# Kernel optimization log

Measured on AMD Instinct MI355X. Metric: run time of the kernel, lower is better.

Reference implementation:

```python
import jax, jax.numpy as jnp
import numpy as np

PHI = (1.0 + float(np.sqrt(5.0))) / 2.0  # golden ratio used by the model


def setup_inputs() -> dict:
    key = jax.random.key(0)
    ks = jax.random.split(key, 12)
    B, S = 4, 1024
    V, D, H, N = 32000, 128, 8, 128
    dh = D // H
    return {
        'input_ids': jax.random.randint(ks[0], (B, S), 0, V),
        'emb': jax.random.normal(ks[1], (V, 2 * D), jnp.float32),
        'w_query': jax.random.normal(ks[2], (H, dh), jnp.float32) * 0.02,
        'b_query': jnp.zeros((H, dh), jnp.float32),
        'w_key': jax.random.normal(ks[3], (H, dh), jnp.float32) * 0.02,
        'b_key': jnp.zeros((H, dh), jnp.float32),
        'W_ctx': jax.random.normal(ks[4], (D, D), jnp.float32) * 0.05,
        'W_res': jax.random.normal(ks[5], (N, D), jnp.float32) * 0.02,
        'B_res': jnp.zeros((N, D), jnp.float32),
        'W_real': jax.random.normal(ks[6], (D, N), jnp.float32) * 0.05,
        'W_imag': jax.random.normal(ks[7], (D, N), jnp.float32) * 0.05,
        'W_out': jax.random.normal(ks[8], (V, D), jnp.float32) * 0.02,
    }


def _forward(input_ids, emb, w_query, b_query, w_key, b_key,
             W_ctx, W_res, B_res, W_real, W_imag, W_out):
    B, S = input_ids.shape
    D = W_ctx.shape[0]
    H, dh = w_query.shape
    e = emb[input_ids]                      # [B,S,2D]
    w_emb, b_emb = e[..., :D], e[..., D:]
    t = jnp.arange(S, dtype=jnp.float32)    # time indices
    tphi = t * PHI

    # --- sequential Euler recurrence (independent of attention) -> states X ---
    def step(carry, xs):
        h_r, h_i = carry
        w_t, b_t, tp = xs                   # w_t,b_t: [B,D]; tp: scalar
        wl = 1.0 + jnp.abs(w_t)
        th_r = h_r / wl + b_t + tp
        th_i = h_i / wl + b_t + tp
        sr, cr = jnp.sin(th_r), jnp.cos(th_r)
        si, ci = jnp.sin(th_i), jnp.cos(th_i)
        new_r = cr * ci - sr * si
        new_i = cr * si + sr * ci
        return (new_r, new_i), new_r + new_i

    init = (jnp.zeros((B, D), e.dtype), jnp.zeros((B, D), e.dtype))
    _, Xs = jax.lax.scan(step, init, (jnp.swapaxes(w_emb, 0, 1),
                                      jnp.swapaxes(b_emb, 0, 1), tphi))
    X = jnp.swapaxes(Xs, 0, 1)              # [B,S,D] cached states

    # --- multi-head Euler-phase attention with strict-causal (exclusive) mask ---
    Xh = X.reshape(B, S, H, dh)
    th_q = Xh / (1.0 + jnp.abs(w_query)) + b_query + tphi[None, :, None, None]
    q = jnp.concatenate([jnp.cos(th_q), jnp.sin(th_q)], axis=-1)   # [B,S,H,2dh]
    th_k = Xh / (1.0 + jnp.abs(w_key)) + b_key                     # keys: no t term
    k = jnp.concatenate([jnp.cos(th_k), jnp.sin(th_k)], axis=-1)
    scores = jnp.einsum('bihd,bjhd->bhij', q, k) / jnp.sqrt(2.0 * dh)
    mask = jnp.tril(jnp.ones((S, S), bool), k=-1)                  # j < i strictly
    scores = jnp.where(mask, scores, -1e9)
    wts = jax.nn.softmax(scores, axis=-1) * mask                   # row 0 -> all-zero
    context = jnp.einsum('bhij,bjd->bid', wts, X)                  # heads summed
    x = X + context @ W_ctx.T

    # --- resonant trig layer ---
    theta = x[:, :, None, :] / (1.0 + jnp.abs(W_res)) + B_res \
            + tphi[None, :, None, None]                            # [B,S,N,D]
    cos_sum = jnp.cos(theta).sum(-1)                               # [B,S,N]
    sin_sum = jnp.sin(theta).sum(-1)
    x = x + jax.nn.silu(cos_sum @ W_real.T + sin_sum @ W_imag.T)

    return x @ W_out.T                                             # [B,S,V]


def reference(input_ids, emb, w_query, b_query, w_key, b_key,
              W_ctx, W_res, B_res, W_real, W_imag, W_out):
    return _forward(input_ids, emb, w_query, b_query, w_key, b_key,
                    W_ctx, W_res, B_res, W_real, W_imag, W_out)
```

## Files before the change

kernel.cpp:

```cpp
#include <hip/hip_runtime.h>


#define DEV static __device__ __forceinline__

typedef __attribute__((ext_vector_type(8))) short short8;
typedef __attribute__((ext_vector_type(4))) float f32x4;

#define INV2PI 0.15915494309189535f
#define INVPI  0.3183098861837907f
#define PHI    1.6180339887498949f
#define SSCALE 0.17677669529663687f

DEV unsigned short f2bf(float x){
  unsigned u = __float_as_uint(x);
  u += 0x7fff + ((u >> 16) & 1);
  return (unsigned short)(u >> 16);
}
DEV float fract1(float x){ return __builtin_amdgcn_fractf(x); }
DEV float sin2pi(float f){ return __builtin_amdgcn_sinf(f); }
DEV float cos2pi(float f){ return __builtin_amdgcn_cosf(f); }
DEV float rcpf_(float x){ return __builtin_amdgcn_rcpf(x); }

DEV void cp16(const float* g, float* l){
  __builtin_amdgcn_global_load_lds(
      (const __attribute__((address_space(1))) unsigned*)g,
      (__attribute__((address_space(3))) unsigned*)l, 16, 0, 0);
}

__global__ __launch_bounds__(256) void k_cast(
    const float* __restrict__ Wctx, const float* __restrict__ Wres,
    const float* __restrict__ Bres, const float* __restrict__ Wreal,
    const float* __restrict__ Wimag, const float* __restrict__ Wout,
    unsigned short* __restrict__ Woutb, unsigned short* __restrict__ Wctxb,
    unsigned short* __restrict__ WriTb, float* __restrict__ raT,
    float* __restrict__ rcT){
  int i = blockIdx.x * 256 + threadIdx.x;
  if (i < 4096000){ Woutb[i] = f2bf(Wout[i]); return; }
  i -= 4096000;
  if (i < 16384){ Wctxb[i] = f2bf(Wctx[i]); return; }
  i -= 16384;
  if (i < 32768){
    int d = i >> 8, kk = i & 255;
    WriTb[i] = f2bf(kk < 128 ? Wreal[d*128 + kk] : Wimag[d*128 + kk - 128]);
    return;
  }
  i -= 32768;
  if (i < 16384){
    int d = i >> 7, n = i & 127;
    raT[i] = INV2PI * rcpf_(1.f + fabsf(Wres[n*128 + d]));
    rcT[i] = Bres[n*128 + d] * INV2PI;
  }
}

__global__ __launch_bounds__(128) void k_prep(const int* __restrict__ ids,
    const float* __restrict__ emb, float* __restrict__ P){
  int bt = blockIdx.x;
  int t  = bt & 1023;
  int d  = threadIdx.x;
  int id = ids[bt];
  float w  = emb[id*256 + d];
  float bb = emb[id*256 + 128 + d];
  float a = INV2PI * rcpf_(1.f + fabsf(w));
  float c = (bb + (float)t * PHI) * INVPI;
  ((float2*)P)[bt*128 + d] = make_float2(a, c);
}

__global__ __launch_bounds__(128) void k_scan(const float* __restrict__ P,
                                              float* __restrict__ X,
                                              unsigned short* __restrict__ XT){
  __shared__ float buf[2][32*256];
  int b  = blockIdx.x;
  int tid = threadIdx.x;
  int wv = tid >> 6, ln = tid & 63;
  const float* Pb = P + (size_t)b * 1024 * 256;
  for (int i = 0; i < 16; i++){
    int o = (i*2 + wv) * 256;
    cp16(Pb + o + ln*4, &buf[0][o]);
  }
  __syncthreads();
  float s = 0.f;
  float* Xb = X + (size_t)b * 1024 * 128;
  unsigned short* XTb = XT + (size_t)(b*128 + tid) * 1024;
  for (int c = 0; c < 32; c++){
    int cur = c & 1;
    if (c + 1 < 32){
      const float* Pn = Pb + (size_t)(c+1) * 8192;
      float* lb = &buf[cur ^ 1][0];
      for (int i = 0; i < 16; i++){
        int o = (i*2 + wv) * 256;
        cp16(Pn + o + ln*4, lb + o);
      }
    }
    const float* bc = &buf[cur][0];
    unsigned pk[16];
    #pragma unroll
    for (int t = 0; t < 32; t++){
      float a  = bc[t*256 + tid*2];
      float cc = bc[t*256 + tid*2 + 1];
      float rev = fmaf(s, a, cc);
      float f = fract1(rev);
      s = sin2pi(f) + cos2pi(f);
      Xb[(c*32 + t)*128 + tid] = s;
      unsigned short h = f2bf(s);
      if (t & 1) pk[t>>1] |= (unsigned)h << 16;
      else       pk[t>>1]  = (unsigned)h;
    }
    uint4* dst = (uint4*)(XTb + c*32);
    #pragma unroll
    for (int i = 0; i < 4; i++)
      dst[i] = make_uint4(pk[i*4+0], pk[i*4+1], pk[i*4+2], pk[i*4+3]);
    __syncthreads();
  }
}

__global__ __launch_bounds__(128) void k_qk(const float* __restrict__ X,
    const float* __restrict__ wq, const float* __restrict__ bq,
    const float* __restrict__ wk, const float* __restrict__ bk,
    unsigned short* __restrict__ q, unsigned short* __restrict__ k){
  int bt = blockIdx.x;
  int t = bt & 1023;
  int tid = threadIdx.x;
  float x = X[(size_t)bt*128 + tid];
  int h = tid >> 4, c = tid & 15;
  size_t base = (size_t)bt*256 + h*32 + c;
  float aq = rcpf_(1.f + fabsf(wq[tid]));
  float fq = fract1(fmaf(x, aq, bq[tid] + (float)t * PHI) * INV2PI);
  q[base]      = f2bf(cos2pi(fq));
  q[base + 16] = f2bf(sin2pi(fq));
  float ak = rcpf_(1.f + fabsf(wk[tid]));
  float fk = fract1(fmaf(x, ak, bk[tid]) * INV2PI);
  k[base]      = f2bf(cos2pi(fk));
  k[base + 16] = f2bf(sin2pi(fk));
}

__global__ __launch_bounds__(256) void k_attn_z(const unsigned short* __restrict__ q,
    const unsigned short* __restrict__ k, float* __restrict__ Z){
  int blk = blockIdx.x;
  int it = blk & 15, h = (blk >> 4) & 7, b = blk >> 7;
  int tid = threadIdx.x, w = tid >> 6, ln = tid & 63;
  int ib = it*64 + w*16;
  short8 qa = *(const short8*)(q + ((size_t)(b*1024 + ib + (ln & 15))*8 + h)*32 + (ln >> 4)*8);
  const unsigned short* kb = k + ((size_t)(b*1024 + (ln & 15))*8 + h)*32 + (ln >> 4)*8;
  float z0 = 0.f, z1 = 0.f, z2 = 0.f, z3 = 0.f;
  int irow = ib + (ln >> 4)*4;
  int jcol = ln & 15;
  for (int jt = 0; jt <= (ib >> 4); jt++){
    short8 kf = *(const short8*)(kb + (size_t)jt*16*256);
    f32x4 c = {0.f, 0.f, 0.f, 0.f};
    c = __builtin_amdgcn_mfma_f32_16x16x32_bf16(qa, kf, c, 0, 0, 0);
    int j = jt*16 + jcol;
    if (j < irow + 0) z0 += __expf(c[0]*SSCALE);
    if (j < irow + 1) z1 += __expf(c[1]*SSCALE);
    if (j < irow + 2) z2 += __expf(c[2]*SSCALE);
    if (j < irow + 3) z3 += __expf(c[3]*SSCALE);
  }
  #pragma unroll
  for (int m = 1; m < 16; m <<= 1){
    z0 += __shfl_xor(z0, m, 64); z1 += __shfl_xor(z1, m, 64);
    z2 += __shfl_xor(z2, m, 64); z3 += __shfl_xor(z3, m, 64);
  }
  if ((ln & 15) == 0){
    float* zp = Z + (size_t)(b*8 + h)*1024 + irow;
    zp[0] = z0; zp[1] = z1; zp[2] = z2; zp[3] = z3;
  }
}

__global__ __launch_bounds__(256) void k_attn_w(const unsigned short* __restrict__ q,
    const unsigned short* __restrict__ k, const float* __restrict__ Z,
    unsigned short* __restrict__ W){
  __shared__ float invZ[8][64];
  int b = blockIdx.x / 136, tr = blockIdx.x % 136;
  int it = 0; while ((it+1)*(it+2)/2 <= tr) it++;
  int jt = tr - it*(it+1)/2;
  int ib = it*64, jb = jt*64;
  int tid = threadIdx.x;
  for (int i = tid; i < 512; i += 256){
    int hh = i >> 6, rr = i & 63;
    float zz = Z[(size_t)(b*8 + hh)*1024 + ib + rr];
    invZ[hh][rr] = zz > 0.f ? rcpf_(zz) : 0.f;
  }
  __syncthreads();
  int w = tid >> 6, ln = tid & 63;
  int iw = ib + w*16;
  int rloc = w*16 + (ln >> 4)*4;
  int irow = iw + (ln >> 4)*4;
  int jcol = ln & 15;
  float acc[4][4] = {};
  for (int h = 0; h < 8; h++){
    short8 qa = *(const short8*)(q + ((size_t)(b*1024 + iw + (ln & 15))*8 + h)*32 + (ln >> 4)*8);
    float iz0 = invZ[h][rloc+0], iz1 = invZ[h][rloc+1];
    float iz2 = invZ[h][rloc+2], iz3 = invZ[h][rloc+3];
    for (int jtt = 0; jtt < 4; jtt++){
      short8 kf = *(const short8*)(k + ((size_t)(b*1024 + jb + jtt*16 + (ln & 15))*8 + h)*32 + (ln >> 4)*8);
      f32x4 c = {0.f, 0.f, 0.f, 0.f};
      c = __builtin_amdgcn_mfma_f32_16x16x32_bf16(qa, kf, c, 0, 0, 0);
      int j = jb + jtt*16 + jcol;
      if (j < irow + 0) acc[jtt][0] += __expf(c[0]*SSCALE)*iz0;
      if (j < irow + 1) acc[jtt][1] += __expf(c[1]*SSCALE)*iz1;
      if (j < irow + 2) acc[jtt][2] += __expf(c[2]*SSCALE)*iz2;
      if (j < irow + 3) acc[jtt][3] += __expf(c[3]*SSCALE)*iz3;
    }
  }
  #pragma unroll
  for (int jtt = 0; jtt < 4; jtt++)
    #pragma unroll
    for (int r = 0; r < 4; r++)
      W[(size_t)(b*1024 + irow + r)*1024 + jb + jtt*16 + jcol] = f2bf(acc[jtt][r]);
}

__global__ __launch_bounds__(256) void k_gemm(const unsigned short* __restrict__ A,
    const unsigned short* __restrict__ B, void* __restrict__ Cv,
    int K, int lda, int ldb, int ldc,
    long Abat, long Bbat, long Cbat, int causal, int obf,
    const float* __restrict__ Xadd){
  int bz = blockIdx.z;
  A += (long)bz * Abat; B += (long)bz * Bbat;
  int tid = threadIdx.x, w = tid >> 6, ln = tid & 63;
  int m0 = blockIdx.x*128 + (w & 1)*64;
  int n0 = blockIdx.y*128 + (w >> 1)*64;
  int kmax = causal ? (blockIdx.x + 1)*128 : K;
  if (kmax > K) kmax = K;
  f32x4 acc[4][4];
  #pragma unroll
  for (int i = 0; i < 4; i++)
    #pragma unroll
    for (int j = 0; j < 4; j++) acc[i][j] = (f32x4){0.f, 0.f, 0.f, 0.f};
  const unsigned short* Ap = A + (long)(m0 + (ln & 15))*lda + (ln >> 4)*8;
  const unsigned short* Bp = B + (long)(n0 + (ln & 15))*ldb + (ln >> 4)*8;
  for (int kb = 0; kb < kmax; kb += 32){
    short8 af[4], bf[4];
    #pragma unroll
    for (int i = 0; i < 4; i++) af[i] = *(const short8*)(Ap + (long)i*16*lda + kb);
    #pragma unroll
    for (int i = 0; i < 4; i++) bf[i] = *(const short8*)(Bp + (long)i*16*ldb + kb);
    #pragma unroll
    for (int i = 0; i < 4; i++)
      #pragma unroll
      for (int j = 0; j < 4; j++)
        acc[i][j] = __builtin_amdgcn_mfma_f32_16x16x32_bf16(af[i], bf[j], acc[i][j], 0, 0, 0);
  }
  int r0 = (ln >> 4)*4, jc = ln & 15;
  if (obf == 1){
    unsigned short* C = (unsigned short*)Cv + (long)bz * Cbat;
    #pragma unroll
    for (int i = 0; i < 4; i++)
      #pragma unroll
      for (int j = 0; j < 4; j++)
        #pragma unroll
        for (int r = 0; r < 4; r++)
          C[(long)(m0 + i*16 + r0 + r)*ldc + n0 + j*16 + jc] = f2bf(acc[i][j][r]);
  } else if (obf == 2){
    unsigned short* C = (unsigned short*)Cv;
    #pragma unroll
    for (int i = 0; i < 4; i++)
      #pragma unroll
      for (int j = 0; j < 4; j++)
        #pragma unroll
        for (int r = 0; r < 4; r++){
          long idx = (long)(m0 + i*16 + r0 + r)*ldc + n0 + j*16 + jc;
          float uu = acc[i][j][r];
          float sig = rcpf_(1.f + __expf(-uu));
          C[idx] = f2bf(Xadd[idx] + uu*sig);
        }
  } else if (obf == 3){
    float* C = (float*)Cv + (long)bz * Cbat;
    #pragma unroll
    for (int i = 0; i < 4; i++)
      #pragma unroll
      for (int j = 0; j < 4; j++)
        #pragma unroll
        for (int r = 0; r < 4; r++)
          __builtin_nontemporal_store(acc[i][j][r],
              C + (long)(m0 + i*16 + r0 + r)*ldc + n0 + j*16 + jc);
  } else {
    float* C = (float*)Cv + (long)bz * Cbat;
    #pragma unroll
    for (int i = 0; i < 4; i++)
      #pragma unroll
      for (int j = 0; j < 4; j++)
        #pragma unroll
        for (int r = 0; r < 4; r++)
          C[(long)(m0 + i*16 + r0 + r)*ldc + n0 + j*16 + jc] = acc[i][j][r];
  }
}

__global__ __launch_bounds__(128) void k_theta(const float* __restrict__ Xf,
    const float* __restrict__ ctx2, const float* __restrict__ raT,
    const float* __restrict__ rcT, float* __restrict__ xout,
    unsigned short* __restrict__ A7){
  __shared__ float xs[8][128];
  int b = blockIdx.x >> 7, sc = blockIdx.x & 127;
  int s0 = sc*8;
  int n = threadIdx.x;
  #pragma unroll
  for (int s = 0; s < 8; s++){
    size_t idx = (size_t)(b*1024 + s0 + s)*128 + n;
    float v = Xf[idx] + ctx2[idx];
    xs[s][n] = v;
    xout[idx] = v;
  }
  __syncthreads();
  float tp[8];
  #pragma unroll
  for (int s = 0; s < 8; s++) tp[s] = (float)(s0 + s) * (float)(PHI * INV2PI);
  float cs[8] = {0,0,0,0,0,0,0,0}, ss[8] = {0,0,0,0,0,0,0,0};
  for (int d = 0; d < 128; d++){
    float a  = raT[d*128 + n];
    float c0 = rcT[d*128 + n];
    #pragma unroll
    for (int s = 0; s < 8; s++){
      float f = fract1(fmaf(xs[s][d], a, c0) + tp[s]);
      cs[s] += cos2pi(f);
      ss[s] += sin2pi(f);
    }
  }
  #pragma unroll
  for (int s = 0; s < 8; s++){
    size_t row = (size_t)(b*1024 + s0 + s);
    A7[row*256 + n]       = f2bf(cs[s]);
    A7[row*256 + 128 + n] = f2bf(ss[s]);
  }
}

extern "C" void kernel_launch(void* const* d_in, const int* in_sizes, int n_in,
                              void* d_out, int out_size, void* d_ws, size_t ws_size,
                              hipStream_t stream){
  const int*   ids  = (const int*)  d_in[0];
  const float* emb  = (const float*)d_in[1];
  const float* wq   = (const float*)d_in[2];
  const float* bq   = (const float*)d_in[3];
  const float* wk   = (const float*)d_in[4];
  const float* bk   = (const float*)d_in[5];
  const float* Wctx = (const float*)d_in[6];
  const float* Wres = (const float*)d_in[7];
  const float* Bres = (const float*)d_in[8];
  const float* Wreal= (const float*)d_in[9];
  const float* Wimag= (const float*)d_in[10];
  const float* Wout = (const float*)d_in[11];

  char* p = (char*)d_ws;
  auto alloc = [&](size_t bytes) -> void* {
    void* r = (void*)p; p += (bytes + 255) & ~(size_t)255; return r;
  };
  float*          P     = (float*)         alloc(4ull*1024*128*2*4);
  float*          X     = (float*)         alloc(4ull*1024*128*4);
  unsigned short* XT    = (unsigned short*)alloc(4ull*128*1024*2);
  unsigned short* q     = (unsigned short*)alloc(4ull*1024*256*2);
  unsigned short* k     = (unsigned short*)alloc(4ull*1024*256*2);
  float*          Z     = (float*)         alloc(4ull*8*1024*4);
  unsigned short* Wsum  = (unsigned short*)alloc(4ull*1024*1024*2);
  unsigned short* tmpb  = (unsigned short*)alloc(4ull*1024*128*2);
  float*          ctx2  = (float*)         alloc(4ull*1024*128*4);
  float*          xout  = (float*)         alloc(4ull*1024*128*4);
  unsigned short* A7    = (unsigned short*)alloc(4096ull*256*2);
  unsigned short* xb    = (unsigned short*)alloc(4096ull*128*2);
  unsigned short* Woutb = (unsigned short*)alloc(32000ull*128*2);
  unsigned short* Wctxb = (unsigned short*)alloc(128ull*128*2);
  unsigned short* WriTb = (unsigned short*)alloc(128ull*256*2);
  float*          raT   = (float*)         alloc(16384ull*4);
  float*          rcT   = (float*)         alloc(16384ull*4);

  hipLaunchKernelGGL(k_cast,  dim3(16256), dim3(256), 0, stream,
                     Wctx, Wres, Bres, Wreal, Wimag, Wout, Woutb, Wctxb, WriTb, raT, rcT);
  hipLaunchKernelGGL(k_prep,  dim3(4096), dim3(128), 0, stream, ids, emb, P);
  hipLaunchKernelGGL(k_scan,  dim3(4),    dim3(128), 0, stream, P, X, XT);
  hipLaunchKernelGGL(k_qk,    dim3(4096), dim3(128), 0, stream, X, wq, bq, wk, bk, q, k);
  hipLaunchKernelGGL(k_attn_z,dim3(512),  dim3(256), 0, stream, q, k, Z);
  hipMemsetAsync(Wsum, 0, 4ull*1024*1024*2, stream);
  hipLaunchKernelGGL(k_attn_w,dim3(544),  dim3(256), 0, stream, q, k, Z, Wsum);
  hipLaunchKernelGGL(k_gemm,  dim3(8,1,4), dim3(256), 0, stream,
                     Wsum, XT, (void*)tmpb, 1024, 1024, 1024, 128,
                     (long)1024*1024, (long)128*1024, (long)1024*128, 1, 1,
                     (const float*)nullptr);
  hipLaunchKernelGGL(k_gemm,  dim3(32,1,1), dim3(256), 0, stream,
                     tmpb, Wctxb, (void*)ctx2, 128, 128, 128, 128,
                     0L, 0L, 0L, 0, 0, (const float*)nullptr);
  hipLaunchKernelGGL(k_theta, dim3(512), dim3(128), 0, stream, X, ctx2, raT, rcT, xout, A7);
  hipLaunchKernelGGL(k_gemm,  dim3(32,1,1), dim3(256), 0, stream,
                     A7, WriTb, (void*)xb, 256, 256, 256, 128,
                     0L, 0L, 0L, 0, 2, xout);
  hipLaunchKernelGGL(k_gemm,  dim3(32,250,1), dim3(256), 0, stream,
                     xb, Woutb, d_out, 128, 128, 128, 32000,
                     0L, 0L, 0L, 0, 3, (const float*)nullptr);
}
```

Baseline: 798.0 us.

## Simplify scan to single sine, fuse prologue kernels, drop Wsum memset

The scan recurrence uses the identity sin+cos = sqrt2*sin(x+pi/4) and folds the sqrt2 and phase offset into the precomputed P coefficients, so each step on the serial critical path evaluates one sine instead of a sine and a cosine. The weight-cast and embedding-prep kernels are merged into one launch. The full memset of the attention weight matrix is replaced by having k_attn_w blocks zero the mirrored upper-triangle tiles. The softmax exponentials switch to exp2f with a prescaled constant. The trig identity changes rounding in the recurrence slightly.

Result: no change. 791.2 us (-0.9%).

```diff
diff --git a/kernel.cpp b/kernel.cpp
--- a/kernel.cpp
+++ b/kernel.cpp
@@ -9,7 +9,9 @@
 #define INV2PI 0.15915494309189535f
 #define INVPI  0.3183098861837907f
 #define PHI    1.6180339887498949f
+#define SQRT2  1.4142135623730951f
 #define SSCALE 0.17677669529663687f
+#define SS2    0.25503471060f
 
 DEV unsigned short f2bf(float x){
   unsigned u = __float_as_uint(x);
@@ -27,42 +29,42 @@
       (__attribute__((address_space(3))) unsigned*)l, 16, 0, 0);
 }
 
-__global__ __launch_bounds__(256) void k_cast(
+__global__ __launch_bounds__(256) void k_prol(
     const float* __restrict__ Wctx, const float* __restrict__ Wres,
     const float* __restrict__ Bres, const float* __restrict__ Wreal,
     const float* __restrict__ Wimag, const float* __restrict__ Wout,
     unsigned short* __restrict__ Woutb, unsigned short* __restrict__ Wctxb,
     unsigned short* __restrict__ WriTb, float* __restrict__ raT,
-    float* __restrict__ rcT){
-  int i = blockIdx.x * 256 + threadIdx.x;
-  if (i < 4096000){ Woutb[i] = f2bf(Wout[i]); return; }
-  i -= 4096000;
-  if (i < 16384){ Wctxb[i] = f2bf(Wctx[i]); return; }
-  i -= 16384;
-  if (i < 32768){
-    int d = i >> 8, kk = i & 255;
-    WriTb[i] = f2bf(kk < 128 ? Wreal[d*128 + kk] : Wimag[d*128 + kk - 128]);
-    return;
-  }
-  i -= 32768;
-  if (i < 16384){
+    float* __restrict__ rcT,
+    const int* __restrict__ ids, const float* __restrict__ emb,
+    float* __restrict__ P){
+  int bx = blockIdx.x;
+  if (bx < 16256){
+    int i = bx * 256 + threadIdx.x;
+    if (i < 4096000){ Woutb[i] = f2bf(Wout[i]); return; }
+    i -= 4096000;
+    if (i < 16384){ Wctxb[i] = f2bf(Wctx[i]); return; }
+    i -= 16384;
+    if (i < 32768){
+      int d = i >> 8, kk = i & 255;
+      WriTb[i] = f2bf(kk < 128 ? Wreal[d*128 + kk] : Wimag[d*128 + kk - 128]);
+      return;
+    }
+    i -= 32768;
     int d = i >> 7, n = i & 127;
     raT[i] = INV2PI * rcpf_(1.f + fabsf(Wres[n*128 + d]));
     rcT[i] = Bres[n*128 + d] * INV2PI;
-  }
-}
-
-__global__ __launch_bounds__(128) void k_prep(const int* __restrict__ ids,
-    const float* __restrict__ emb, float* __restrict__ P){
-  int bt = blockIdx.x;
+    return;
+  }
+  int bt = (bx - 16256)*2 + (threadIdx.x >> 7);
   int t  = bt & 1023;
-  int d  = threadIdx.x;
+  int d  = threadIdx.x & 127;
   int id = ids[bt];
   float w  = emb[id*256 + d];
   float bb = emb[id*256 + 128 + d];
-  float a = INV2PI * rcpf_(1.f + fabsf(w));
-  float c = (bb + (float)t * PHI) * INVPI;
-  ((float2*)P)[bt*128 + d] = make_float2(a, c);
+  float a2 = SQRT2 * INV2PI * rcpf_(1.f + fabsf(w));
+  float c2 = (bb + (float)t * PHI) * INVPI + 0.125f;
+  ((float2*)P)[bt*128 + d] = make_float2(a2, c2);
 }
 
 __global__ __launch_bounds__(128) void k_scan(const float* __restrict__ P,
@@ -78,7 +80,7 @@
     cp16(Pb + o + ln*4, &buf[0][o]);
   }
   __syncthreads();
-  float s = 0.f;
+  float u = 0.f;
   float* Xb = X + (size_t)b * 1024 * 128;
   unsigned short* XTb = XT + (size_t)(b*128 + tid) * 1024;
   for (int c = 0; c < 32; c++){
@@ -97,9 +99,9 @@
     for (int t = 0; t < 32; t++){
       float a  = bc[t*256 + tid*2];
       float cc = bc[t*256 + tid*2 + 1];
-      float rev = fmaf(s, a, cc);
-      float f = fract1(rev);
-      s = sin2pi(f) + cos2pi(f);
+      float f = fract1(fmaf(u, a, cc));
+      u = sin2pi(f);
+      float s = u * SQRT2;
       Xb[(c*32 + t)*128 + tid] = s;
       unsigned short h = f2bf(s);
       if (t & 1) pk[t>>1] |= (unsigned)h << 16;
@@ -149,10 +151,10 @@
     f32x4 c = {0.f, 0.f, 0.f, 0.f};
     c = __builtin_amdgcn_mfma_f32_16x16x32_bf16(qa, kf, c, 0, 0, 0);
     int j = jt*16 + jcol;
-    if (j < irow + 0) z0 += __expf(c[0]*SSCALE);
-    if (j < irow + 1) z1 += __expf(c[1]*SSCALE);
-    if (j < irow + 2) z2 += __expf(c[2]*SSCALE);
-    if (j < irow + 3) z3 += __expf(c[3]*SSCALE);
+    if (j < irow + 0) z0 += exp2f(c[0]*SS2);
+    if (j < irow + 1) z1 += exp2f(c[1]*SS2);
+    if (j < irow + 2) z2 += exp2f(c[2]*SS2);
+    if (j < irow + 3) z3 += exp2f(c[3]*SS2);
   }
   #pragma unroll
   for (int m = 1; m < 16; m <<= 1){
@@ -174,6 +176,15 @@
   int jt = tr - it*(it+1)/2;
   int ib = it*64, jb = jt*64;
   int tid = threadIdx.x;
+  if (it != jt){
+    uint4 z4 = make_uint4(0u, 0u, 0u, 0u);
+    int idx = tid*2;
+    #pragma unroll
+    for (int s = 0; s < 2; s++, idx++){
+      int row = idx >> 3, c4 = idx & 7;
+      *(uint4*)(W + (size_t)(b*1024 + jb + row)*1024 + ib + c4*8) = z4;
+    }
+  }
   for (int i = tid; i < 512; i += 256){
     int hh = i >> 6, rr = i & 63;
     float zz = Z[(size_t)(b*8 + hh)*1024 + ib + rr];
@@ -195,10 +206,10 @@
       f32x4 c = {0.f, 0.f, 0.f, 0.f};
       c = __builtin_amdgcn_mfma_f32_16x16x32_bf16(qa, kf, c, 0, 0, 0);
       int j = jb + jtt*16 + jcol;
-      if (j < irow + 0) acc[jtt][0] += __expf(c[0]*SSCALE)*iz0;
-      if (j < irow + 1) acc[jtt][1] += __expf(c[1]*SSCALE)*iz1;
-      if (j < irow + 2) acc[jtt][2] += __expf(c[2]*SSCALE)*iz2;
-      if (j < irow + 3) acc[jtt][3] += __expf(c[3]*SSCALE)*iz3;
+      if (j < irow + 0) acc[jtt][0] += exp2f(c[0]*SS2)*iz0;
+      if (j < irow + 1) acc[jtt][1] += exp2f(c[1]*SS2)*iz1;
+      if (j < irow + 2) acc[jtt][2] += exp2f(c[2]*SS2)*iz2;
+      if (j < irow + 3) acc[jtt][3] += exp2f(c[3]*SS2)*iz3;
     }
   }
   #pragma unroll
@@ -360,13 +371,12 @@
   float*          raT   = (float*)         alloc(16384ull*4);
   float*          rcT   = (float*)         alloc(16384ull*4);
 
-  hipLaunchKernelGGL(k_cast,  dim3(16256), dim3(256), 0, stream,
-                     Wctx, Wres, Bres, Wreal, Wimag, Wout, Woutb, Wctxb, WriTb, raT, rcT);
-  hipLaunchKernelGGL(k_prep,  dim3(4096), dim3(128), 0, stream, ids, emb, P);
+  hipLaunchKernelGGL(k_prol,  dim3(18304), dim3(256), 0, stream,
+                     Wctx, Wres, Bres, Wreal, Wimag, Wout, Woutb, Wctxb, WriTb, raT, rcT,
+                     ids, emb, P);
   hipLaunchKernelGGL(k_scan,  dim3(4),    dim3(128), 0, stream, P, X, XT);
   hipLaunchKernelGGL(k_qk,    dim3(4096), dim3(128), 0, stream, X, wq, bq, wk, bk, q, k);
   hipLaunchKernelGGL(k_attn_z,dim3(512),  dim3(256), 0, stream, q, k, Z);
-  hipMemsetAsync(Wsum, 0, 4ull*1024*1024*2, stream);
   hipLaunchKernelGGL(k_attn_w,dim3(544),  dim3(256), 0, stream, q, k, Z, Wsum);
   hipLaunchKernelGGL(k_gemm,  dim3(8,1,4), dim3(256), 0, stream,
                      Wsum, XT, (void*)tmpb, 1024, 1024, 1024, 128,
```
